# Optimization experiments

Hardware: AMD Instinct MI355X
Metric: run time of the kernel (lower is better)

Reference implementation:

```python
import jax, jax.numpy as jnp
import numpy as np

SEQ, BS, IN, HS = 512, 64, 1024, 1024


def _xavier(key, shape):
    fan_in, fan_out = shape
    limit = np.sqrt(6.0 / (fan_in + fan_out)).astype(np.float32)
    return jax.random.uniform(key, shape, jnp.float32, -limit, limit)


def setup_inputs() -> dict:
    key = jax.random.key(0)
    k1, k2, k3, k4, k5 = jax.random.split(key, 5)
    return {
        "x": jax.random.normal(k1, (SEQ, BS, IN), jnp.float32),
        "h0": jax.random.normal(k2, (1, BS, HS), jnp.float32),
        "c0": jax.random.normal(k3, (1, BS, HS), jnp.float32),
        "weight_ih": _xavier(k4, (IN, 4 * HS)),
        "weight_hh": _xavier(k5, (HS, 4 * HS)),
        "bias": jnp.zeros((4 * HS,), jnp.float32),
    }


def reference(x, h0, c0, weight_ih, weight_hh, bias):
    HSd = weight_hh.shape[0]
    # Precompute the input projection for all timesteps in one big GEMM.
    x_gates = jnp.einsum('sbi,ih->sbh', x, weight_ih) + bias  # [S, B, 4H]

    def step(carry, xg_t):
        h_t, c_t = carry
        gates = xg_t + h_t @ weight_hh  # [B, 4H]
        i_t = jax.nn.sigmoid(gates[:, :HSd])
        f_t = jax.nn.sigmoid(gates[:, HSd:2 * HSd])
        g_t = jnp.tanh(gates[:, 2 * HSd:3 * HSd])
        o_t = jax.nn.sigmoid(gates[:, 3 * HSd:])
        c_t = f_t * c_t + i_t * g_t
        h_t = o_t * jnp.tanh(c_t)
        return (h_t, c_t), h_t

    (h_T, c_T), hidden_seq = jax.lax.scan(step, (h0[0], c0[0]), x_gates)
    return hidden_seq, (h_T[None], c_T[None])
```

## Files before the change

kernel.cpp:

```cpp
#include <hip/hip_runtime.h>
#include <stdint.h>


typedef unsigned short u16;
typedef __attribute__((ext_vector_type(8))) short bf16x8;
typedef __attribute__((ext_vector_type(2))) uint64_t u64x2;
typedef __attribute__((ext_vector_type(4))) float f32x4;

#define BAR_LDS()                                        \
  do {                                                   \
    __builtin_amdgcn_sched_barrier(0);                   \
    asm volatile("s_waitcnt lgkmcnt(0)" ::: "memory");   \
    __builtin_amdgcn_s_barrier();                        \
    __builtin_amdgcn_sched_barrier(0);                   \
  } while (0)

static __device__ __forceinline__ u16 f2b(float f) {
  uint32_t b = __float_as_uint(f);
  return (u16)((b + 0x7fffu + ((b >> 16) & 1u)) >> 16);
}
static __device__ __forceinline__ uint64_t pack4(float4 v) {
  return (uint64_t)f2b(v.x) | ((uint64_t)f2b(v.y) << 16) |
         ((uint64_t)f2b(v.z) << 32) | ((uint64_t)f2b(v.w) << 48);
}
static __device__ __forceinline__ float b2f(u16 u) {
  return __uint_as_float(((uint32_t)u) << 16);
}
static __device__ __forceinline__ float sigm(float x) {
  return 1.0f / (1.0f + __expf(-x));
}
static __device__ __forceinline__ float tanh_(float x) {
  float e = __expf(2.0f * x);
  return 1.0f - 2.0f / (e + 1.0f);
}

__global__ __launch_bounds__(256) void transpose_w(const float* __restrict__ Wih,
                                                   const float* __restrict__ Whh,
                                                   u16* __restrict__ Tih,
                                                   u16* __restrict__ Thh) {
  __shared__ float tile[64][65];
  const float* src = blockIdx.z ? Whh : Wih;
  u16* dst = blockIdx.z ? Thh : Tih;
  int k0 = blockIdx.y * 64, n0 = blockIdx.x * 64;
  int tid = threadIdx.x;
#pragma unroll
  for (int i = 0; i < 16; ++i) {
    int idx = i * 256 + tid;
    int kl = idx >> 6, nl = idx & 63;
    tile[kl][nl] = src[(size_t)(k0 + kl) * 4096 + n0 + nl];
  }
  __syncthreads();
#pragma unroll
  for (int i = 0; i < 16; ++i) {
    int idx = i * 256 + tid;
    int nl = idx >> 6, kl = idx & 63;
    dst[(size_t)(n0 + nl) * 1024 + k0 + kl] = f2b(tile[kl][nl]);
  }
}

__global__ __launch_bounds__(256) void convert_h0(const float* __restrict__ h0,
                                                  uint64_t* __restrict__ dst) {
  int i = blockIdx.x * 256 + threadIdx.x;
  float2 v = ((const float2*)h0)[i];
  uint32_t pair = (uint32_t)f2b(v.x) | ((uint32_t)f2b(v.y) << 16);
  dst[i] = (uint64_t)pair;
}

__global__ __launch_bounds__(256) void gemm_xg(const float* __restrict__ A,
                                               const u16* __restrict__ Bt,
                                               const float* __restrict__ bias,
                                               u16* __restrict__ C) {
  __shared__ u16 sA[2][128 * 32];
  __shared__ u16 sB[2][128 * 32];
  const int tid = threadIdx.x;
  const int wave = tid >> 6, lane = tid & 63;
  const int bx = blockIdx.x, by = blockIdx.y;
  const int wr = wave >> 1, wc = wave & 1;
  const int lm = lane & 15, ko = (lane >> 4) * 8;

  const int ar = lane >> 1, ac = (lane & 1) * 16;
  const float* gA = A + (size_t)(by * 128 + wave * 32 + ar) * 1024 + ac;
  const u16* gB = Bt + (size_t)(bx * 128 + wave * 32 + (lane >> 2)) * 1024 + (lane & 3) * 8;
  const int bidx = wave * 1024 + (lane >> 2) * 32 + (lane & 3) * 8;

  f32x4 acc[4][4] = {};

  auto stage = [&](int kt, int buf) {
    const u16* gb = gB + kt * 32;
    bf16x8 b0 = *(const bf16x8*)gb;
    bf16x8 b1 = *(const bf16x8*)(gb + 16 * 1024);
    *(bf16x8*)&sB[buf][bidx] = b0;
    *(bf16x8*)&sB[buf][bidx + 512] = b1;
    const float* ga = gA + kt * 32;
    float4 v0 = *(const float4*)(ga + 0);
    float4 v1 = *(const float4*)(ga + 4);
    float4 v2 = *(const float4*)(ga + 8);
    float4 v3 = *(const float4*)(ga + 12);
    uint64_t* la = (uint64_t*)&sA[buf][wave * 1024 + ar * 32 + ac];
    la[0] = pack4(v0);
    la[1] = pack4(v1);
    la[2] = pack4(v2);
    la[3] = pack4(v3);
  };

  stage(0, 0);
  __syncthreads();
  int p = 0;
  for (int kt = 0; kt < 32; ++kt) {
    if (kt < 31) stage(kt + 1, p ^ 1);
    bf16x8 af[4], bfv[4];
#pragma unroll
    for (int i = 0; i < 4; ++i)
      af[i] = *(const bf16x8*)&sA[p][(wr * 64 + i * 16 + lm) * 32 + ko];
#pragma unroll
    for (int j = 0; j < 4; ++j)
      bfv[j] = *(const bf16x8*)&sB[p][(wc * 64 + j * 16 + lm) * 32 + ko];
#pragma unroll
    for (int i = 0; i < 4; ++i)
#pragma unroll
      for (int j = 0; j < 4; ++j)
        acc[i][j] = __builtin_amdgcn_mfma_f32_16x16x32_bf16(af[i], bfv[j], acc[i][j], 0, 0, 0);
    __syncthreads();
    p ^= 1;
  }

  float bj[4];
#pragma unroll
  for (int j = 0; j < 4; ++j)
    bj[j] = bias[bx * 128 + wc * 64 + j * 16 + lm];
#pragma unroll
  for (int i = 0; i < 4; ++i) {
    int row = by * 128 + wr * 64 + i * 16 + (lane >> 4) * 4;
#pragma unroll
    for (int j = 0; j < 4; ++j) {
      int col = bx * 128 + wc * 64 + j * 16 + lm;
#pragma unroll
      for (int r = 0; r < 4; ++r)
        C[(size_t)(row + r) * 4096 + col] = f2b(acc[i][j][r] + bj[j]);
    }
  }
}

__global__ __launch_bounds__(512, 1) void recur_pers(
    const u16* __restrict__ xg,
    const u16* __restrict__ whh_t,
    uint64_t* __restrict__ h_tag,
    float* __restrict__ c_st,
    float* __restrict__ out_h,
    float* __restrict__ out_hT, float* __restrict__ out_cT,
    int t0, int W) {
  __shared__ float xchg[8][16][68];

  const int tid = threadIdx.x;
  const int wave = tid >> 6, lane = tid & 63;
  const int bid = blockIdx.x;
  const int un = bid & 63;
  const int bq = bid >> 6;
  const int lm = lane & 15, hi = lane >> 4;

  bf16x8 bfr[4][4];
#pragma unroll
  for (int nt = 0; nt < 4; ++nt) {
    const u16* bp = whh_t + (size_t)(nt * 1024 + un * 16 + lm) * 1024 + wave * 128 + hi * 8;
#pragma unroll
    for (int kk = 0; kk < 4; ++kk) bfr[kk][nt] = *(const bf16x8*)(bp + kk * 32);
  }

  const int r_b = tid >> 4, u = tid & 15;
  const int b = bq * 16 + r_b;
  const int unit = un * 16 + u;
  float c_val = (tid < 256) ? c_st[b * 1024 + unit] : 0.f;

  const int b_row = bq * 16 + lm;

  for (int ts = 0; ts < W; ++ts) {
    const int t = t0 + ts;

    u16 xr0 = 0, xr1 = 0, xr2 = 0, xr3 = 0;
    if (tid < 256) {
      const u16* xgp = xg + ((size_t)ts * 64 + b) * 4096 + unit;
      xr0 = xgp[0];
      xr1 = xgp[1024];
      xr2 = xgp[2048];
      xr3 = xgp[3072];
    }

    const uint64_t* hb = h_tag + ((size_t)((t - 1) & 1) * 64 + b_row) * 512 +
                         wave * 64 + hi * 4;
    uint64_t wbuf[16];
    {
      uint32_t spin = 0;
      bool ok = false;
      for (; spin < (1u << 15); ++spin) {
#pragma unroll
        for (int kk = 0; kk < 4; ++kk)
#pragma unroll
          for (int j = 0; j < 4; ++j)
            wbuf[kk * 4 + j] = __hip_atomic_load(hb + kk * 16 + j, __ATOMIC_RELAXED,
                                                 __HIP_MEMORY_SCOPE_AGENT);
        bool good = true;
#pragma unroll
        for (int i = 0; i < 16; ++i)
          good &= ((uint32_t)(wbuf[i] >> 32) >= (uint32_t)t);
        if (__all(good)) { ok = true; break; }
        __builtin_amdgcn_s_sleep(1);
      }
      if (!ok && lane == 0)
        out_h[(size_t)t * 65536 + bid] = 1.0e6f;
    }

    f32x4 acc[4] = {};
#pragma unroll
    for (int kk = 0; kk < 4; ++kk) {
      u64x2 v;
      v.x = (uint64_t)(uint32_t)wbuf[kk * 4 + 0] |
            ((uint64_t)(uint32_t)wbuf[kk * 4 + 1] << 32);
      v.y = (uint64_t)(uint32_t)wbuf[kk * 4 + 2] |
            ((uint64_t)(uint32_t)wbuf[kk * 4 + 3] << 32);
      bf16x8 a = __builtin_bit_cast(bf16x8, v);
#pragma unroll
      for (int nt = 0; nt < 4; ++nt)
        acc[nt] = __builtin_amdgcn_mfma_f32_16x16x32_bf16(a, bfr[kk][nt], acc[nt], 0, 0, 0);
    }
    {
      int crow = hi * 4;
#pragma unroll
      for (int nt = 0; nt < 4; ++nt)
#pragma unroll
        for (int r = 0; r < 4; ++r) xchg[wave][crow + r][nt * 16 + lm] = acc[nt][r];
    }
    BAR_LDS();

    if (tid < 256) {
      float raw[4];
#pragma unroll
      for (int g = 0; g < 4; ++g) {
        int c = g * 16 + u;
        float s = xchg[0][r_b][c];
#pragma unroll
        for (int w = 1; w < 8; ++w) s += xchg[w][r_b][c];
        raw[g] = s;
      }
      float ig = sigm(raw[0] + b2f(xr0));
      float fg = sigm(raw[1] + b2f(xr1));
      float gg = tanh_(raw[2] + b2f(xr2));
      float og = sigm(raw[3] + b2f(xr3));
      c_val = fg * c_val + ig * gg;
      float h_new = og * tanh_(c_val);
      uint32_t mine = f2b(h_new);
      uint32_t other = __shfl_xor(mine, 1);
      if ((u & 1) == 0) {
        uint64_t word = (uint64_t)(mine | (other << 16)) | ((uint64_t)(uint32_t)(t + 1) << 32);
        __hip_atomic_store(
            h_tag + ((size_t)(t & 1) * 64 + b) * 512 + (unit >> 1), word,
            __ATOMIC_RELAXED, __HIP_MEMORY_SCOPE_AGENT);
      }
      out_h[(size_t)t * 65536 + (size_t)b * 1024 + unit] = h_new;
      if (t == 511) {
        out_hT[b * 1024 + unit] = h_new;
        out_cT[b * 1024 + unit] = c_val;
      }
    }
    BAR_LDS();
  }

  if (tid < 256) c_st[b * 1024 + unit] = c_val;
}

extern "C" void kernel_launch(void* const* d_in, const int* in_sizes, int n_in,
                              void* d_out, int out_size, void* d_ws, size_t ws_size,
                              hipStream_t stream) {
  const float* x = (const float*)d_in[0];
  const float* h0 = (const float*)d_in[1];
  const float* c0 = (const float*)d_in[2];
  const float* wih = (const float*)d_in[3];
  const float* whh = (const float*)d_in[4];
  const float* bias = (const float*)d_in[5];

  float* out = (float*)d_out;
  float* out_h = out;
  float* out_hT = out + (size_t)512 * 64 * 1024;
  float* out_cT = out_hT + 64 * 1024;

  const size_t fixed = (size_t)2 * 4096 * 1024 * 2
                       + (size_t)2 * 64 * 512 * 8
                       + (size_t)64 * 1024 * 4;
  int W = 64;
  while (W > 4 && fixed + (size_t)W * 64 * 4096 * 2 > ws_size) W >>= 2;

  char* ws = (char*)d_ws;
  u16* wih_t = (u16*)ws;     ws += (size_t)4096 * 1024 * 2;
  u16* whh_t = (u16*)ws;     ws += (size_t)4096 * 1024 * 2;
  u16* xg = (u16*)ws;        ws += (size_t)W * 64 * 4096 * 2;
  uint64_t* h_tag = (uint64_t*)ws; ws += (size_t)2 * 64 * 512 * 8;
  float* c_st = (float*)ws;

  hipMemsetAsync(h_tag, 0, (size_t)2 * 64 * 512 * 8, stream);
  convert_h0<<<128, 256, 0, stream>>>(h0, h_tag + (size_t)64 * 512);
  hipMemcpyAsync(c_st, c0, (size_t)64 * 1024 * 4, hipMemcpyDeviceToDevice, stream);
  transpose_w<<<dim3(64, 16, 2), 256, 0, stream>>>(wih, whh, wih_t, whh_t);

  for (int t0 = 0; t0 < 512; t0 += W) {
    gemm_xg<<<dim3(32, W / 2), 256, 0, stream>>>(x + (size_t)t0 * 64 * 1024, wih_t, bias, xg);
    int t0c = t0, Wc = W;
    void* args[] = {(void*)&xg,    (void*)&whh_t,  (void*)&h_tag, (void*)&c_st,
                    (void*)&out_h, (void*)&out_hT, (void*)&out_cT,
                    (void*)&t0c,   (void*)&Wc};
    hipLaunchCooperativeKernel((const void*)recur_pers, dim3(256), dim3(512), args, 0,
                               stream);
  }
}
```

Measured before the change: 4.024 ms.

## Fuse next-window input GEMM and x conversion into persistent recurrence kernel

When the workspace is large enough, the input-projection GEMM for the next 64-step window runs inside the persistent recurrent kernel. Each timestep does half of a small MFMA tile with its otherwise idle compute, and results go into double-buffered xg buffers. The kernel also converts a later x window to bf16 in the background, so the separate gemm_xg launches between windows go away. This hides the GEMM behind the latency-bound recurrence, at the cost of extra work and memory traffic inside each step, which may lengthen the critical path.

```diff
diff --git a/kernel.cpp b/kernel.cpp
--- a/kernel.cpp
+++ b/kernel.cpp
@@ -64,6 +64,13 @@
   float2 v = ((const float2*)h0)[i];
   uint32_t pair = (uint32_t)f2b(v.x) | ((uint32_t)f2b(v.y) << 16);
   dst[i] = (uint64_t)pair;
+}
+
+__global__ __launch_bounds__(256) void convert_xwin(const float* __restrict__ src,
+                                                    u16* __restrict__ dst) {
+  int i = blockIdx.x * 256 + threadIdx.x;
+  float2 v = ((const float2*)src)[i];
+  ((uint32_t*)dst)[i] = (uint32_t)f2b(v.x) | ((uint32_t)f2b(v.y) << 16);
 }
 
 __global__ __launch_bounds__(256) void gemm_xg(const float* __restrict__ A,
@@ -148,7 +155,13 @@
     float* __restrict__ c_st,
     float* __restrict__ out_h,
     float* __restrict__ out_hT, float* __restrict__ out_cT,
-    int t0, int W) {
+    int t0, int W,
+    u16* __restrict__ xg_wr,
+    const u16* __restrict__ x_rd,
+    const u16* __restrict__ wih_t,
+    const float* __restrict__ bias,
+    const float* __restrict__ xcv_src,
+    u16* __restrict__ xcv_dst) {
   __shared__ float xchg[8][16][68];
 
   const int tid = threadIdx.x;
@@ -172,6 +185,9 @@
   float c_val = (tid < 256) ? c_st[b * 1024 + unit] : 0.f;
 
   const int b_row = bq * 16 + lm;
+
+  const int rt = bid >> 3, ct = bid & 7;
+  f32x4 gacc0 = {}, gacc1 = {};
 
   for (int ts = 0; ts < W; ++ts) {
     const int t = t0 + ts;
@@ -261,6 +277,38 @@
         out_cT[b * 1024 + unit] = c_val;
       }
     }
+
+    if (xg_wr) {
+      const int p2 = ts >> 1, half = ts & 1;
+      const int id = p2 * 8 + wave;
+      const int rsub = rt * 128 + (id >> 5) * 16;
+      const int gcol = ct * 512 + (id & 31) * 16 + lm;
+      const u16* ax = x_rd + (size_t)(rsub + lm) * 1024 + half * 512 + hi * 8;
+      const u16* bw = wih_t + (size_t)gcol * 1024 + half * 512 + hi * 8;
+      if (!half) { gacc0 = (f32x4){}; gacc1 = (f32x4){}; }
+#pragma unroll
+      for (int kk = 0; kk < 16; kk += 2) {
+        bf16x8 a0 = *(const bf16x8*)(ax + kk * 32);
+        bf16x8 b0 = *(const bf16x8*)(bw + kk * 32);
+        bf16x8 a1 = *(const bf16x8*)(ax + (kk + 1) * 32);
+        bf16x8 b1 = *(const bf16x8*)(bw + (kk + 1) * 32);
+        gacc0 = __builtin_amdgcn_mfma_f32_16x16x32_bf16(a0, b0, gacc0, 0, 0, 0);
+        gacc1 = __builtin_amdgcn_mfma_f32_16x16x32_bf16(a1, b1, gacc1, 0, 0, 0);
+      }
+      if (half) {
+        float bj = bias[gcol];
+        f32x4 s = gacc0 + gacc1;
+        int crow = rsub + hi * 4;
+#pragma unroll
+        for (int r = 0; r < 4; ++r)
+          xg_wr[(size_t)(crow + r) * 4096 + gcol] = f2b(s[r] + bj);
+      }
+    }
+    if (xcv_src && !(ts & 1)) {
+      int idx = bid * 16384 + (ts >> 1) * 512 + tid;
+      xcv_dst[idx] = f2b(xcv_src[idx]);
+    }
+
     BAR_LDS();
   }
 
@@ -282,31 +330,75 @@
   float* out_hT = out + (size_t)512 * 64 * 1024;
   float* out_cT = out_hT + 64 * 1024;
 
-  const size_t fixed = (size_t)2 * 4096 * 1024 * 2
-                       + (size_t)2 * 64 * 512 * 8
-                       + (size_t)64 * 1024 * 4;
-  int W = 64;
-  while (W > 4 && fixed + (size_t)W * 64 * 4096 * 2 > ws_size) W >>= 2;
+  const size_t MB = 1024 * 1024;
+  const size_t fused_need = 16 * MB
+                            + 64 * MB
+                            + 16 * MB
+                            + (size_t)2 * 64 * 512 * 8
+                            + (size_t)64 * 1024 * 4;
+  const bool fused = ws_size >= fused_need;
 
   char* ws = (char*)d_ws;
-  u16* wih_t = (u16*)ws;     ws += (size_t)4096 * 1024 * 2;
-  u16* whh_t = (u16*)ws;     ws += (size_t)4096 * 1024 * 2;
-  u16* xg = (u16*)ws;        ws += (size_t)W * 64 * 4096 * 2;
-  uint64_t* h_tag = (uint64_t*)ws; ws += (size_t)2 * 64 * 512 * 8;
-  float* c_st = (float*)ws;
-
-  hipMemsetAsync(h_tag, 0, (size_t)2 * 64 * 512 * 8, stream);
-  convert_h0<<<128, 256, 0, stream>>>(h0, h_tag + (size_t)64 * 512);
-  hipMemcpyAsync(c_st, c0, (size_t)64 * 1024 * 4, hipMemcpyDeviceToDevice, stream);
-  transpose_w<<<dim3(64, 16, 2), 256, 0, stream>>>(wih, whh, wih_t, whh_t);
-
-  for (int t0 = 0; t0 < 512; t0 += W) {
-    gemm_xg<<<dim3(32, W / 2), 256, 0, stream>>>(x + (size_t)t0 * 64 * 1024, wih_t, bias, xg);
-    int t0c = t0, Wc = W;
-    void* args[] = {(void*)&xg,    (void*)&whh_t,  (void*)&h_tag, (void*)&c_st,
-                    (void*)&out_h, (void*)&out_hT, (void*)&out_cT,
-                    (void*)&t0c,   (void*)&Wc};
-    hipLaunchCooperativeKernel((const void*)recur_pers, dim3(256), dim3(512), args, 0,
-                               stream);
-  }
-}
+  u16* wih_t = (u16*)ws;   ws += (size_t)4096 * 1024 * 2;
+  u16* whh_t = (u16*)ws;   ws += (size_t)4096 * 1024 * 2;
+
+  if (fused) {
+    u16* xgA = (u16*)ws;   ws += (size_t)64 * 64 * 4096 * 2;
+    u16* xgB = (u16*)ws;   ws += (size_t)64 * 64 * 4096 * 2;
+    u16* xb0 = (u16*)ws;   ws += (size_t)64 * 64 * 1024 * 2;
+    u16* xb1 = (u16*)ws;   ws += (size_t)64 * 64 * 1024 * 2;
+    uint64_t* h_tag = (uint64_t*)ws; ws += (size_t)2 * 64 * 512 * 8;
+    float* c_st = (float*)ws;
+
+    hipMemsetAsync(h_tag, 0, (size_t)2 * 64 * 512 * 8, stream);
+    convert_h0<<<128, 256, 0, stream>>>(h0, h_tag + (size_t)64 * 512);
+    hipMemcpyAsync(c_st, c0, (size_t)64 * 1024 * 4, hipMemcpyDeviceToDevice, stream);
+    transpose_w<<<dim3(64, 16, 2), 256, 0, stream>>>(wih, whh, wih_t, whh_t);
+    convert_xwin<<<8192, 256, 0, stream>>>(x + (size_t)64 * 65536, xb1);
+    gemm_xg<<<dim3(32, 32), 256, 0, stream>>>(x, wih_t, bias, xgA);
+
+    for (int w = 0; w < 8; ++w) {
+      int t0 = w * 64, Wc = 64;
+      const u16* xg_rd = (w & 1) ? xgB : xgA;
+      u16* xg_w = (w < 7) ? ((w & 1) ? xgA : xgB) : nullptr;
+      const u16* x_rd = ((w + 1) & 1) ? xb1 : xb0;
+      const float* xcv_s = (w < 6) ? (x + (size_t)(t0 + 128) * 65536) : nullptr;
+      u16* xcv_d = (w & 1) ? xb1 : xb0;
+      void* args[] = {(void*)&xg_rd, (void*)&whh_t, (void*)&h_tag, (void*)&c_st,
+                      (void*)&out_h, (void*)&out_hT, (void*)&out_cT,
+                      (void*)&t0,    (void*)&Wc,
+                      (void*)&xg_w,  (void*)&x_rd,  (void*)&wih_t, (void*)&bias,
+                      (void*)&xcv_s, (void*)&xcv_d};
+      hipLaunchCooperativeKernel((const void*)recur_pers, dim3(256), dim3(512), args, 0,
+                                 stream);
+    }
+  } else {
+    int W = 64;
+    const size_t fixed = 16 * MB + (size_t)2 * 64 * 512 * 8 + (size_t)64 * 1024 * 4;
+    while (W > 4 && fixed + (size_t)W * 64 * 4096 * 2 > ws_size) W >>= 2;
+    u16* xg = (u16*)ws;    ws += (size_t)W * 64 * 4096 * 2;
+    uint64_t* h_tag = (uint64_t*)ws; ws += (size_t)2 * 64 * 512 * 8;
+    float* c_st = (float*)ws;
+
+    hipMemsetAsync(h_tag, 0, (size_t)2 * 64 * 512 * 8, stream);
+    convert_h0<<<128, 256, 0, stream>>>(h0, h_tag + (size_t)64 * 512);
+    hipMemcpyAsync(c_st, c0, (size_t)64 * 1024 * 4, hipMemcpyDeviceToDevice, stream);
+    transpose_w<<<dim3(64, 16, 2), 256, 0, stream>>>(wih, whh, wih_t, whh_t);
+
+    for (int t0 = 0; t0 < 512; t0 += W) {
+      gemm_xg<<<dim3(32, W / 2), 256, 0, stream>>>(x + (size_t)t0 * 64 * 1024, wih_t, bias, xg);
+      int t0c = t0, Wc = W;
+      u16* xg_w = nullptr;
+      const u16* x_rd = nullptr;
+      const float* xcv_s = nullptr;
+      u16* xcv_d = nullptr;
+      void* args[] = {(void*)&xg,    (void*)&whh_t, (void*)&h_tag, (void*)&c_st,
+                      (void*)&out_h, (void*)&out_hT, (void*)&out_cT,
+                      (void*)&t0c,   (void*)&Wc,
+                      (void*)&xg_w,  (void*)&x_rd,  (void*)&wih_t, (void*)&bias,
+                      (void*)&xcv_s, (void*)&xcv_d};
+      hipLaunchCooperativeKernel((const void*)recur_pers, dim3(256), dim3(512), args, 0,
+                                 stream);
+    }
+  }
+}
```

After: 5.965 ms. 1.48x slower.
